# Performance work log

Hardware: AMD Instinct MI355X
Metric: run time of the kernel (lower is better)

Reference implementation:

```python
import jax, jax.numpy as jnp
import numpy as np

B, N, E = 4, 50000, 800000
C_IN, C_OUT, OUT = 64, 64, 32


def _uniform(key, shape, fan_in):
    s = 1.0 / np.sqrt(fan_in)
    return jax.random.uniform(key, shape, jnp.float32, -s, s)


def setup_inputs() -> dict:
    key = jax.random.key(0)
    ks = jax.random.split(key, 16)
    x = jax.random.normal(ks[0], (B, N, C_IN), jnp.float32)
    edge_index = jax.random.randint(ks[1], (2, E), 0, N, jnp.int64)
    edge_weight = jax.random.uniform(ks[2], (E,), jnp.float32)
    # GCNConv weights (in->out) and biases for z, r, h gates
    Wz = _uniform(ks[3], (C_IN, C_OUT), C_IN); bz = jnp.zeros((C_OUT,), jnp.float32)
    Wr = _uniform(ks[4], (C_IN, C_OUT), C_IN); br = jnp.zeros((C_OUT,), jnp.float32)
    Wh = _uniform(ks[5], (C_IN, C_OUT), C_IN); bh = jnp.zeros((C_OUT,), jnp.float32)
    # gating Linears: (2*out -> out)
    Lz = _uniform(ks[6], (2 * C_OUT, C_OUT), 2 * C_OUT); Lzb = _uniform(ks[7], (C_OUT,), 2 * C_OUT)
    Lr = _uniform(ks[8], (2 * C_OUT, C_OUT), 2 * C_OUT); Lrb = _uniform(ks[9], (C_OUT,), 2 * C_OUT)
    Lh = _uniform(ks[10], (2 * C_OUT, C_OUT), 2 * C_OUT); Lhb = _uniform(ks[11], (C_OUT,), 2 * C_OUT)
    # output head Linear(out_channels -> out_size)
    Hw = _uniform(ks[12], (C_OUT, OUT), C_OUT); Hb = _uniform(ks[13], (OUT,), C_OUT)
    return dict(x=x, edge_index=edge_index, edge_weight=edge_weight,
                Wz=Wz, bz=bz, Wr=Wr, br=br, Wh=Wh, bh=bh,
                Lz=Lz, Lzb=Lzb, Lr=Lr, Lrb=Lrb, Lh=Lh, Lhb=Lhb,
                Hw=Hw, Hb=Hb)


def _gcn(x, W, b, src, tgt, norm):
    # x: (B, N, Cin) -> (B, N, Cout); sym-normalized aggregation over edges
    xw = jnp.einsum('bnf,fo->bno', x, W)
    msg = xw[:, src] * norm[None, :, None]          # (B, E+N, Cout)
    agg = jnp.zeros_like(xw).at[:, tgt].add(msg)    # scatter-add at targets
    return agg + b


def reference(x, edge_index, edge_weight, Wz, bz, Wr, br, Wh, bh,
              Lz, Lzb, Lr, Lrb, Lh, Lhb, Hw, Hb):
    src, tgt = edge_index[0], edge_index[1]
    loop = jnp.arange(N)
    src_f = jnp.concatenate([src, loop])
    tgt_f = jnp.concatenate([tgt, loop])
    w_f = jnp.concatenate([edge_weight, jnp.ones((N,), edge_weight.dtype)])
    deg = jnp.zeros((N,), w_f.dtype).at[tgt_f].add(w_f)  # self-loops => deg >= 1
    dinv = jax.lax.rsqrt(deg)
    norm = dinv[src_f] * w_f * dinv[tgt_f]
    H = jnp.zeros((x.shape[0], N, Wz.shape[1]), x.dtype)  # TGCN2 initial hidden state
    gz = _gcn(x, Wz, bz, src_f, tgt_f, norm)
    Z = jax.nn.sigmoid(jnp.concatenate([gz, H], -1) @ Lz + Lzb)
    gr = _gcn(x, Wr, br, src_f, tgt_f, norm)
    R = jax.nn.sigmoid(jnp.concatenate([gr, H], -1) @ Lr + Lrb)
    gh = _gcn(x, Wh, bh, src_f, tgt_f, norm)
    Ht = jnp.tanh(jnp.concatenate([gh, H * R], -1) @ Lh + Lhb)
    Hn = Z * H + (1.0 - Z) * Ht
    return jax.nn.relu(Hn) @ Hw + Hb
```

## Files before the change

### kernel.cpp

```cpp
#include <hip/hip_runtime.h>
#include <stdint.h>

#define N_NODES 50000
#define N_EDGES 800000
#define XSTRIDE 3200000
#define PS      3200000
#define PSU     1600000
#define EBLK    3125
#define XPBLK   12500
#define FUSE_T  15730
#define MAXDEG  64
#define CSH     24
#define WMASK   0xFFFFFFu

typedef __attribute__((ext_vector_type(8))) short short8;
typedef __attribute__((ext_vector_type(4))) float float4v;

static __device__ __forceinline__ unsigned f2bf(float f) {
  unsigned u = __float_as_uint(f);
  return (u + 0x7fffu + ((u >> 16) & 1u)) >> 16;
}
static __device__ __forceinline__ float bflo(unsigned u) { return __uint_as_float(u << 16); }
static __device__ __forceinline__ float bfhi(unsigned u) { return __uint_as_float(u & 0xffff0000u); }
static __device__ __forceinline__ float dinv_of(unsigned pk) {
  return rsqrtf(1.0f + (float)(pk & WMASK) * 0x1p-18f);
}

__global__ __launch_bounds__(256) void kfused(
    const float* __restrict__ x, uint2* __restrict__ xp,
    const int* __restrict__ tgt, const int* __restrict__ src,
    const float* __restrict__ ew,
    unsigned* __restrict__ packed32, int2* __restrict__ colw,
    const float* __restrict__ Wz, const float* __restrict__ bz,
    const float* __restrict__ Wh, const float* __restrict__ bh,
    const float* __restrict__ Lz, const float* __restrict__ Lzb,
    const float* __restrict__ Lh, const float* __restrict__ Lhb,
    const float* __restrict__ Hw,
    ushort* __restrict__ BG, ushort* __restrict__ BH, float* __restrict__ czh) {
  int blk = blockIdx.x;
  if (blk % 5 == 0) {
    int eb = blk / 5;
    if (eb >= EBLK) return;
    int e = eb * 256 + threadIdx.x;
    int t = tgt[e], s = src[e];
    t = t < 0 ? 0 : (t >= N_NODES ? N_NODES - 1 : t);
    s = s < 0 ? 0 : (s >= N_NODES ? N_NODES - 1 : s);
    float wv = ew[e];
    wv = wv < 0.f ? 0.f : wv;
    unsigned fix = (unsigned)(wv * 262144.0f);
    fix = fix > 262143u ? 262143u : fix;
    unsigned old = atomicAdd(&packed32[t], (1u << CSH) | fix);
    unsigned rank = old >> CSH;
    if (rank < MAXDEG)
      colw[t * MAXDEG + (int)rank] = make_int2(s, __float_as_int(wv));
    return;
  }
  int j = blk - blk / 5 - 1;
  if (j < XPBLK) {
    int i = j * 256 + threadIdx.x;
    float v0 = x[i];
    float v1 = x[i + XSTRIDE];
    float v2 = x[i + 2 * XSTRIDE];
    float v3 = x[i + 3 * XSTRIDE];
    uint2 u;
    u.x = (f2bf(v1) << 16) | f2bf(v0);
    u.y = (f2bf(v3) << 16) | f2bf(v2);
    xp[i] = u;
    return;
  }
  int idx = (j - XPBLK) * 256 + threadIdx.x;
  if (idx < 16384) {
    int i = idx & 7, lane = (idx >> 3) & 63, kk = (idx >> 9) & 1;
    int jt = (idx >> 10) & 7, hilo = idx >> 13;
    int c = kk * 32 + ((lane >> 4) << 3) + i;
    int jj0 = jt * 16 + (lane & 15);
    const float* W = (jj0 < 64) ? Wz : Wh;
    const float* L = (jj0 < 64) ? Lz : Lh;
    int jj = jj0 & 63;
    float v = 0.f;
    #pragma unroll 8
    for (int k = 0; k < 64; ++k) v += W[c * 64 + k] * L[k * 64 + jj];
    unsigned hi = f2bf(v);
    BG[idx] = hilo ? (ushort)f2bf(v - bflo(hi)) : (ushort)hi;
  } else if (idx < 20480) {
    int t = idx - 16384;
    int i = t & 7, lane = (t >> 3) & 63, kk = (t >> 9) & 1;
    int ot = (t >> 10) & 1, hilo = (t >> 11) & 1;
    int c = kk * 32 + ((lane >> 4) << 3) + i;
    int o = ot * 16 + (lane & 15);
    float v = Hw[c * 32 + o];
    unsigned hi = f2bf(v);
    BH[t] = hilo ? (ushort)f2bf(v - bflo(hi)) : (ushort)hi;
  } else if (idx < 20608) {
    int jj0 = idx - 20480;
    int jj = jj0 & 63;
    const float* L  = (jj0 < 64) ? Lz  : Lh;
    const float* bb = (jj0 < 64) ? bz  : bh;
    const float* Lb = (jj0 < 64) ? Lzb : Lhb;
    float v = Lb[jj];
    #pragma unroll 8
    for (int k = 0; k < 64; ++k) v += bb[k] * L[k * 64 + jj];
    czh[jj0] = v;
  }
}

__global__ __launch_bounds__(256) void kagg(
    const uint4* __restrict__ xp4, const unsigned* __restrict__ packed32,
    const int4* __restrict__ colw4, unsigned* __restrict__ aggp32) {
  int lane = threadIdx.x & 63;
  int w = threadIdx.x >> 6;
  int n = blockIdx.x * 4 + w;
  int c2 = lane & 31;
  int eh = lane >> 5;
  unsigned pk = packed32[n];
  int cnt = (int)(pk >> CSH);
  cnt = cnt > MAXDEG ? MAXDEG : cnt;
  float dinv_n = dinv_of(pk);
  float a0, a1, a2, a3, b0, b1, b2, b3;
  {
    float g = eh ? 0.0f : dinv_n;
    uint4 q = xp4[(size_t)n * 32 + c2];
    a0 = g * bflo(q.x); a1 = g * bfhi(q.x);
    a2 = g * bflo(q.y); a3 = g * bfhi(q.y);
    b0 = g * bflo(q.z); b1 = g * bfhi(q.z);
    b2 = g * bflo(q.w); b3 = g * bfhi(q.w);
  }
  const int4* row = colw4 + (size_t)n * (MAXDEG / 2);
  const int2* row2 = (const int2*)row;
  int p = 0;
  for (; p + 8 <= cnt; p += 8) {
    int4 m0 = row[(p >> 1) + 2 * eh];
    int4 m1 = row[(p >> 1) + 2 * eh + 1];
    float w0 = __int_as_float(m0.y) * dinv_of(packed32[m0.x]);
    float w1 = __int_as_float(m0.w) * dinv_of(packed32[m0.z]);
    float w2 = __int_as_float(m1.y) * dinv_of(packed32[m1.x]);
    float w3 = __int_as_float(m1.w) * dinv_of(packed32[m1.z]);
    uint4 q0 = xp4[(size_t)m0.x * 32 + c2];
    uint4 q1 = xp4[(size_t)m0.z * 32 + c2];
    uint4 q2 = xp4[(size_t)m1.x * 32 + c2];
    uint4 q3 = xp4[(size_t)m1.z * 32 + c2];
    a0 += w0*bflo(q0.x) + w1*bflo(q1.x) + w2*bflo(q2.x) + w3*bflo(q3.x);
    a1 += w0*bfhi(q0.x) + w1*bfhi(q1.x) + w2*bfhi(q2.x) + w3*bfhi(q3.x);
    a2 += w0*bflo(q0.y) + w1*bflo(q1.y) + w2*bflo(q2.y) + w3*bflo(q3.y);
    a3 += w0*bfhi(q0.y) + w1*bfhi(q1.y) + w2*bfhi(q2.y) + w3*bfhi(q3.y);
    b0 += w0*bflo(q0.z) + w1*bflo(q1.z) + w2*bflo(q2.z) + w3*bflo(q3.z);
    b1 += w0*bfhi(q0.z) + w1*bfhi(q1.z) + w2*bfhi(q2.z) + w3*bfhi(q3.z);
    b2 += w0*bflo(q0.w) + w1*bflo(q1.w) + w2*bflo(q2.w) + w3*bflo(q3.w);
    b3 += w0*bfhi(q0.w) + w1*bfhi(q1.w) + w2*bfhi(q2.w) + w3*bfhi(q3.w);
  }
  for (; p + 2 <= cnt; p += 2) {
    int2 m = row2[p + eh];
    float wv = __int_as_float(m.y) * dinv_of(packed32[m.x]);
    uint4 q = xp4[(size_t)m.x * 32 + c2];
    a0 += wv * bflo(q.x); a1 += wv * bfhi(q.x);
    a2 += wv * bflo(q.y); a3 += wv * bfhi(q.y);
    b0 += wv * bflo(q.z); b1 += wv * bfhi(q.z);
    b2 += wv * bflo(q.w); b3 += wv * bfhi(q.w);
  }
  if (p < cnt) {
    int2 m = row2[p];
    float wv = eh ? 0.0f : __int_as_float(m.y) * dinv_of(packed32[m.x]);
    uint4 q = xp4[(size_t)m.x * 32 + c2];
    a0 += wv * bflo(q.x); a1 += wv * bfhi(q.x);
    a2 += wv * bflo(q.y); a3 += wv * bfhi(q.y);
    b0 += wv * bflo(q.z); b1 += wv * bfhi(q.z);
    b2 += wv * bflo(q.w); b3 += wv * bfhi(q.w);
  }
  a0 += __shfl_xor(a0, 32, 64); a1 += __shfl_xor(a1, 32, 64);
  a2 += __shfl_xor(a2, 32, 64); a3 += __shfl_xor(a3, 32, 64);
  b0 += __shfl_xor(b0, 32, 64); b1 += __shfl_xor(b1, 32, 64);
  b2 += __shfl_xor(b2, 32, 64); b3 += __shfl_xor(b3, 32, 64);
  float pa = dinv_n * (eh ? a2 : a0), pb = dinv_n * (eh ? b2 : b0);
  float qa = dinv_n * (eh ? a3 : a1), qb = dinv_n * (eh ? b3 : b1);
  unsigned vlo = f2bf(pa) | (f2bf(pb) << 16);
  unsigned vhi = f2bf(qa) | (f2bf(qb) << 16);
  size_t base = (size_t)(eh * 2) * PSU + (size_t)n * 32 + c2;
  aggp32[base]       = vlo;
  aggp32[base + PSU] = vhi;
}

__global__ __launch_bounds__(256) void kdense(
    const ushort* __restrict__ aggp,
    const ushort* __restrict__ BG, const ushort* __restrict__ BH,
    const float* __restrict__ czh, const float* __restrict__ Hb,
    float* __restrict__ out) {
  __shared__ uint4 sBGv[2048];
  __shared__ uint4 sBHv[512];
  __shared__ float sCzh[128];
  __shared__ float sHb[32];
  __shared__ uint4 sRv[4][128];

  int tid = threadIdx.x;
  {
    const uint4* g = (const uint4*)BG;
    for (int i = tid; i < 2048; i += 256) sBGv[i] = g[i];
    const uint4* g2 = (const uint4*)BH;
    for (int i = tid; i < 512; i += 256) sBHv[i] = g2[i];
    if (tid < 128) sCzh[tid] = czh[tid];
    if (tid < 32) sHb[tid] = Hb[tid];
  }
  __syncthreads();

  int lane = tid & 63;
  int w = tid >> 6;
  const short8* bgf = (const short8*)sBGv;
  const short8* bhf = (const short8*)sBHv;
  char* rbase = (char*)(&sRv[w][0]);
  int rowg = (lane >> 4) * 4;
  int colb = lane & 15;

  #pragma unroll 1
  for (int it = 0; it < 5; ++it) {
    int tile = (it * 625 + blockIdx.x) * 4 + w;
    int b = tile / 3125;
    int n0 = (tile - b * 3125) * 16;

    const ushort* ap = aggp + (size_t)b * PS + (size_t)(n0 + (lane & 15)) * 64
                       + ((lane >> 4) << 3);
    short8 a0 = *(const short8*)(ap);
    short8 a1 = *(const short8*)(ap + 32);

    float4v acc[8];
    #pragma unroll
    for (int jt = 0; jt < 8; ++jt) {
      float bias = sCzh[jt * 16 + (lane & 15)];
      acc[jt] = (float4v){bias, bias, bias, bias};
    }
    #pragma unroll
    for (int hilo = 0; hilo < 2; ++hilo) {
      #pragma unroll
      for (int jt = 0; jt < 8; ++jt) {
        short8 b0 = bgf[((hilo * 8 + jt) * 2 + 0) * 64 + lane];
        short8 b1 = bgf[((hilo * 8 + jt) * 2 + 1) * 64 + lane];
        acc[jt] = __builtin_amdgcn_mfma_f32_16x16x32_bf16(a0, b0, acc[jt], 0, 0, 0);
        acc[jt] = __builtin_amdgcn_mfma_f32_16x16x32_bf16(a1, b1, acc[jt], 0, 0, 0);
      }
    }

    #pragma unroll
    for (int jt = 0; jt < 4; ++jt) {
      #pragma unroll
      for (int r = 0; r < 4; ++r) {
        float z = acc[jt][r], h = acc[jt + 4][r];
        float s = 1.f / (1.f + __expf(-z));
        float e = __expf(2.f * h);
        float t = (e - 1.f) / (e + 1.f);
        float rr = (1.f - s) * t;
        rr = rr > 0.f ? rr : 0.f;
        int row = rowg + r;
        int colx = jt * 16 + colb;
        int byte = (row * 128 + colx * 2) ^ ((row & 7) << 4);
        *(ushort*)(rbase + byte) = (ushort)f2bf(rr);
      }
    }
    __syncthreads();

    short8 ra0, ra1;
    {
      int row = lane & 15;
      int g = (lane >> 4) << 4;
      int swz = (row & 7) << 4;
      ra0 = *(const short8*)(rbase + row * 128 + ((g) ^ swz));
      ra1 = *(const short8*)(rbase + row * 128 + ((64 + g) ^ swz));
    }
    float4v hacc[2];
    #pragma unroll
    for (int ot = 0; ot < 2; ++ot) {
      float hb = sHb[ot * 16 + (lane & 15)];
      hacc[ot] = (float4v){hb, hb, hb, hb};
    }
    #pragma unroll
    for (int hilo = 0; hilo < 2; ++hilo) {
      #pragma unroll
      for (int ot = 0; ot < 2; ++ot) {
        short8 b0 = bhf[((hilo * 2 + ot) * 2 + 0) * 64 + lane];
        short8 b1 = bhf[((hilo * 2 + ot) * 2 + 1) * 64 + lane];
        hacc[ot] = __builtin_amdgcn_mfma_f32_16x16x32_bf16(ra0, b0, hacc[ot], 0, 0, 0);
        hacc[ot] = __builtin_amdgcn_mfma_f32_16x16x32_bf16(ra1, b1, hacc[ot], 0, 0, 0);
      }
    }
    float* ob = out + ((size_t)b * N_NODES + n0) * 32;
    #pragma unroll
    for (int ot = 0; ot < 2; ++ot) {
      #pragma unroll
      for (int r = 0; r < 4; ++r) {
        int row = rowg + r;
        int o = ot * 16 + (lane & 15);
        ob[row * 32 + o] = hacc[ot][r];
      }
    }
    __syncthreads();
  }
}

extern "C" void kernel_launch(void* const* d_in, const int* in_sizes, int n_in,
                              void* d_out, int out_size, void* d_ws, size_t ws_size,
                              hipStream_t stream) {
  const float* x   = (const float*)d_in[0];
  const int*   ei  = (const int*)d_in[1];
  const float* ew  = (const float*)d_in[2];
  const float* Wz  = (const float*)d_in[3];
  const float* bz  = (const float*)d_in[4];
  const float* Wh  = (const float*)d_in[7];
  const float* bh  = (const float*)d_in[8];
  const float* Lz  = (const float*)d_in[9];
  const float* Lzb = (const float*)d_in[10];
  const float* Lh  = (const float*)d_in[13];
  const float* Lhb = (const float*)d_in[14];
  const float* Hw  = (const float*)d_in[15];
  const float* Hb  = (const float*)d_in[16];
  float* out = (float*)d_out;

  const int* src = ei;
  const int* tgt = ei + N_EDGES;

  char* ws = (char*)d_ws;
  ws = (char*)(((uintptr_t)ws + 255) & ~(uintptr_t)255);
  unsigned* packed32 = (unsigned*)ws; ws += (size_t)N_NODES * 4;
  ws = (char*)(((uintptr_t)ws + 255) & ~(uintptr_t)255);
  int2* colw = (int2*)ws;      ws += (size_t)N_NODES * MAXDEG * 8;
  ushort* BG    = (ushort*)ws; ws += 16384 * 2;
  ushort* BH    = (ushort*)ws; ws += 4096 * 2;
  float* czh    = (float*)ws;  ws += 128 * 4;
  ws = (char*)(((uintptr_t)ws + 255) & ~(uintptr_t)255);
  uint2* xp     = (uint2*)ws;  ws += (size_t)N_NODES * 64 * 8;
  unsigned* aggp32 = (unsigned*)ws; ws += (size_t)4 * PSU * 4;

  hipMemsetAsync(packed32, 0, (size_t)N_NODES * 4, stream);
  kfused<<<FUSE_T, 256, 0, stream>>>(
      x, xp, tgt, src, ew, packed32, colw,
      Wz, bz, Wh, bh, Lz, Lzb, Lh, Lhb, Hw, BG, BH, czh);
  kagg<<<N_NODES / 4, 256, 0, stream>>>((const uint4*)xp, packed32,
                                        (const int4*)colw, aggp32);
  kdense<<<625, 256, 0, stream>>>((const ushort*)aggp32, BG, BH, czh, Hb, out);
}
```

Measured before the change: 144.5 us.

## Slice node features into channel planes and gather 16 edges per wave

The packed bf16 features are rewritten into 8 channel-slice planes, so each aggregation block touches only one slice, a smaller gather footprint. The neighbour list is compressed to 4 bytes per edge: a 16-bit source index plus an fp16 weight. The aggregation kernel becomes a grid-stride loop in which each wave processes 16 edges at a time with 4 lanes per edge, reduced by xor shuffles. The aim is better cache locality and fewer index bytes, at the cost of more loop iterations and shuffles per node and reduced precision for edge weights.

```diff
diff --git a/kernel.cpp b/kernel.cpp
--- a/kernel.cpp
+++ b/kernel.cpp
@@ -1,4 +1,5 @@
 #include <hip/hip_runtime.h>
+#include <hip/hip_fp16.h>
 #include <stdint.h>
 
 #define N_NODES 50000
@@ -12,6 +13,10 @@
 #define MAXDEG  64
 #define CSH     24
 #define WMASK   0xFFFFFFu
+#define PLANE2  400000
+#define PLANE4  200000
+#define KAGG_B  12496
+#define WPS     6248
 
 typedef __attribute__((ext_vector_type(8))) short short8;
 typedef __attribute__((ext_vector_type(4))) float float4v;
@@ -27,10 +32,10 @@
 }
 
 __global__ __launch_bounds__(256) void kfused(
-    const float* __restrict__ x, uint2* __restrict__ xp,
+    const float* __restrict__ x, uint2* __restrict__ xps2,
     const int* __restrict__ tgt, const int* __restrict__ src,
     const float* __restrict__ ew,
-    unsigned* __restrict__ packed32, int2* __restrict__ colw,
+    unsigned* __restrict__ packed32, unsigned* __restrict__ colw,
     const float* __restrict__ Wz, const float* __restrict__ bz,
     const float* __restrict__ Wh, const float* __restrict__ bh,
     const float* __restrict__ Lz, const float* __restrict__ Lzb,
@@ -51,13 +56,16 @@
     fix = fix > 262143u ? 262143u : fix;
     unsigned old = atomicAdd(&packed32[t], (1u << CSH) | fix);
     unsigned rank = old >> CSH;
-    if (rank < MAXDEG)
-      colw[t * MAXDEG + (int)rank] = make_int2(s, __float_as_int(wv));
+    if (rank < MAXDEG) {
+      unsigned hb = (unsigned)__half_as_ushort(__float2half(wv));
+      colw[t * MAXDEG + (int)rank] = (hb << 16) | (unsigned)s;
+    }
     return;
   }
   int j = blk - blk / 5 - 1;
   if (j < XPBLK) {
     int i = j * 256 + threadIdx.x;
+    int n = i >> 6, ch = i & 63;
     float v0 = x[i];
     float v1 = x[i + XSTRIDE];
     float v2 = x[i + 2 * XSTRIDE];
@@ -65,7 +73,7 @@
     uint2 u;
     u.x = (f2bf(v1) << 16) | f2bf(v0);
     u.y = (f2bf(v3) << 16) | f2bf(v2);
-    xp[i] = u;
+    xps2[(ch >> 3) * PLANE2 + n * 8 + (ch & 7)] = u;
     return;
   }
   int idx = (j - XPBLK) * 256 + threadIdx.x;
@@ -105,78 +113,64 @@
 }
 
 __global__ __launch_bounds__(256) void kagg(
-    const uint4* __restrict__ xp4, const unsigned* __restrict__ packed32,
-    const int4* __restrict__ colw4, unsigned* __restrict__ aggp32) {
+    const uint4* __restrict__ xps4, const unsigned* __restrict__ packed32,
+    const unsigned* __restrict__ colw, unsigned* __restrict__ aggp32) {
   int lane = threadIdx.x & 63;
-  int w = threadIdx.x >> 6;
-  int n = blockIdx.x * 4 + w;
-  int c2 = lane & 31;
-  int eh = lane >> 5;
-  unsigned pk = packed32[n];
-  int cnt = (int)(pk >> CSH);
-  cnt = cnt > MAXDEG ? MAXDEG : cnt;
-  float dinv_n = dinv_of(pk);
-  float a0, a1, a2, a3, b0, b1, b2, b3;
-  {
-    float g = eh ? 0.0f : dinv_n;
-    uint4 q = xp4[(size_t)n * 32 + c2];
-    a0 = g * bflo(q.x); a1 = g * bfhi(q.x);
-    a2 = g * bflo(q.y); a3 = g * bfhi(q.y);
-    b0 = g * bflo(q.z); b1 = g * bfhi(q.z);
-    b2 = g * bflo(q.w); b3 = g * bfhi(q.w);
-  }
-  const int4* row = colw4 + (size_t)n * (MAXDEG / 2);
-  const int2* row2 = (const int2*)row;
-  int p = 0;
-  for (; p + 8 <= cnt; p += 8) {
-    int4 m0 = row[(p >> 1) + 2 * eh];
-    int4 m1 = row[(p >> 1) + 2 * eh + 1];
-    float w0 = __int_as_float(m0.y) * dinv_of(packed32[m0.x]);
-    float w1 = __int_as_float(m0.w) * dinv_of(packed32[m0.z]);
-    float w2 = __int_as_float(m1.y) * dinv_of(packed32[m1.x]);
-    float w3 = __int_as_float(m1.w) * dinv_of(packed32[m1.z]);
-    uint4 q0 = xp4[(size_t)m0.x * 32 + c2];
-    uint4 q1 = xp4[(size_t)m0.z * 32 + c2];
-    uint4 q2 = xp4[(size_t)m1.x * 32 + c2];
-    uint4 q3 = xp4[(size_t)m1.z * 32 + c2];
-    a0 += w0*bflo(q0.x) + w1*bflo(q1.x) + w2*bflo(q2.x) + w3*bflo(q3.x);
-    a1 += w0*bfhi(q0.x) + w1*bfhi(q1.x) + w2*bfhi(q2.x) + w3*bfhi(q3.x);
-    a2 += w0*bflo(q0.y) + w1*bflo(q1.y) + w2*bflo(q2.y) + w3*bflo(q3.y);
-    a3 += w0*bfhi(q0.y) + w1*bfhi(q1.y) + w2*bfhi(q2.y) + w3*bfhi(q3.y);
-    b0 += w0*bflo(q0.z) + w1*bflo(q1.z) + w2*bflo(q2.z) + w3*bflo(q3.z);
-    b1 += w0*bfhi(q0.z) + w1*bfhi(q1.z) + w2*bfhi(q2.z) + w3*bfhi(q3.z);
-    b2 += w0*bflo(q0.w) + w1*bflo(q1.w) + w2*bflo(q2.w) + w3*bflo(q3.w);
-    b3 += w0*bfhi(q0.w) + w1*bfhi(q1.w) + w2*bfhi(q2.w) + w3*bfhi(q3.w);
-  }
-  for (; p + 2 <= cnt; p += 2) {
-    int2 m = row2[p + eh];
-    float wv = __int_as_float(m.y) * dinv_of(packed32[m.x]);
-    uint4 q = xp4[(size_t)m.x * 32 + c2];
-    a0 += wv * bflo(q.x); a1 += wv * bfhi(q.x);
-    a2 += wv * bflo(q.y); a3 += wv * bfhi(q.y);
-    b0 += wv * bflo(q.z); b1 += wv * bfhi(q.z);
-    b2 += wv * bflo(q.w); b3 += wv * bfhi(q.w);
-  }
-  if (p < cnt) {
-    int2 m = row2[p];
-    float wv = eh ? 0.0f : __int_as_float(m.y) * dinv_of(packed32[m.x]);
-    uint4 q = xp4[(size_t)m.x * 32 + c2];
-    a0 += wv * bflo(q.x); a1 += wv * bfhi(q.x);
-    a2 += wv * bflo(q.y); a3 += wv * bfhi(q.y);
-    b0 += wv * bflo(q.z); b1 += wv * bfhi(q.z);
-    b2 += wv * bflo(q.w); b3 += wv * bfhi(q.w);
-  }
-  a0 += __shfl_xor(a0, 32, 64); a1 += __shfl_xor(a1, 32, 64);
-  a2 += __shfl_xor(a2, 32, 64); a3 += __shfl_xor(a3, 32, 64);
-  b0 += __shfl_xor(b0, 32, 64); b1 += __shfl_xor(b1, 32, 64);
-  b2 += __shfl_xor(b2, 32, 64); b3 += __shfl_xor(b3, 32, 64);
-  float pa = dinv_n * (eh ? a2 : a0), pb = dinv_n * (eh ? b2 : b0);
-  float qa = dinv_n * (eh ? a3 : a1), qb = dinv_n * (eh ? b3 : b1);
-  unsigned vlo = f2bf(pa) | (f2bf(pb) << 16);
-  unsigned vhi = f2bf(qa) | (f2bf(qb) << 16);
-  size_t base = (size_t)(eh * 2) * PSU + (size_t)n * 32 + c2;
-  aggp32[base]       = vlo;
-  aggp32[base + PSU] = vhi;
+  int wid = threadIdx.x >> 6;
+  int slice = blockIdx.x & 7;
+  int wave = (blockIdx.x >> 3) * 4 + wid;
+  int g = lane >> 2, q = lane & 3;
+  const uint4* plane = xps4 + (size_t)slice * PLANE4;
+
+  for (int n = wave; n < N_NODES; n += WPS) {
+    unsigned pk = packed32[n];
+    int cnt = (int)(pk >> CSH);
+    cnt = cnt > MAXDEG ? MAXDEG : cnt;
+    float dinv_n = dinv_of(pk);
+    float a0, a1, a2, a3, b0, b1, b2, b3;
+    {
+      float g0 = (g == 0) ? dinv_n : 0.0f;
+      uint4 qv = plane[n * 4 + q];
+      a0 = g0 * bflo(qv.x); a1 = g0 * bfhi(qv.x);
+      a2 = g0 * bflo(qv.y); a3 = g0 * bfhi(qv.y);
+      b0 = g0 * bflo(qv.z); b1 = g0 * bfhi(qv.z);
+      b2 = g0 * bflo(qv.w); b3 = g0 * bfhi(qv.w);
+    }
+    for (int c0 = 0; c0 < cnt; c0 += 16) {
+      int e = c0 + g;
+      bool valid = e < cnt;
+      unsigned m = valid ? __builtin_nontemporal_load(&colw[n * MAXDEG + e]) : 0u;
+      int s = (int)(m & 0xFFFFu);
+      float wv = 0.0f;
+      if (valid) {
+        wv = __half2float(__ushort_as_half((unsigned short)(m >> 16)))
+             * dinv_of(packed32[s]);
+      }
+      uint4 qv = plane[(size_t)s * 4 + q];
+      a0 += wv * bflo(qv.x); a1 += wv * bfhi(qv.x);
+      a2 += wv * bflo(qv.y); a3 += wv * bfhi(qv.y);
+      b0 += wv * bflo(qv.z); b1 += wv * bfhi(qv.z);
+      b2 += wv * bflo(qv.w); b3 += wv * bfhi(qv.w);
+    }
+    #pragma unroll
+    for (int mask = 4; mask <= 32; mask <<= 1) {
+      a0 += __shfl_xor(a0, mask, 64); a1 += __shfl_xor(a1, mask, 64);
+      a2 += __shfl_xor(a2, mask, 64); a3 += __shfl_xor(a3, mask, 64);
+      b0 += __shfl_xor(b0, mask, 64); b1 += __shfl_xor(b1, mask, 64);
+      b2 += __shfl_xor(b2, mask, 64); b3 += __shfl_xor(b3, mask, 64);
+    }
+    if (lane < 16) {
+      int p = lane >> 2;
+      float ea, eb;
+      if      (p == 0) { ea = a0; eb = b0; }
+      else if (p == 1) { ea = a1; eb = b1; }
+      else if (p == 2) { ea = a2; eb = b2; }
+      else             { ea = a3; eb = b3; }
+      ea *= dinv_n; eb *= dinv_n;
+      aggp32[(size_t)p * PSU + n * 32 + slice * 4 + q] =
+          f2bf(ea) | (f2bf(eb) << 16);
+    }
+  }
 }
 
 __global__ __launch_bounds__(256) void kdense(
@@ -318,19 +312,18 @@
   ws = (char*)(((uintptr_t)ws + 255) & ~(uintptr_t)255);
   unsigned* packed32 = (unsigned*)ws; ws += (size_t)N_NODES * 4;
   ws = (char*)(((uintptr_t)ws + 255) & ~(uintptr_t)255);
-  int2* colw = (int2*)ws;      ws += (size_t)N_NODES * MAXDEG * 8;
+  unsigned* colw = (unsigned*)ws; ws += (size_t)N_NODES * MAXDEG * 4;
   ushort* BG    = (ushort*)ws; ws += 16384 * 2;
   ushort* BH    = (ushort*)ws; ws += 4096 * 2;
   float* czh    = (float*)ws;  ws += 128 * 4;
   ws = (char*)(((uintptr_t)ws + 255) & ~(uintptr_t)255);
-  uint2* xp     = (uint2*)ws;  ws += (size_t)N_NODES * 64 * 8;
+  uint2* xps    = (uint2*)ws;  ws += (size_t)N_NODES * 64 * 8;
   unsigned* aggp32 = (unsigned*)ws; ws += (size_t)4 * PSU * 4;
 
   hipMemsetAsync(packed32, 0, (size_t)N_NODES * 4, stream);
   kfused<<<FUSE_T, 256, 0, stream>>>(
-      x, xp, tgt, src, ew, packed32, colw,
+      x, xps, tgt, src, ew, packed32, colw,
       Wz, bz, Wh, bh, Lz, Lzb, Lh, Lhb, Hw, BG, BH, czh);
-  kagg<<<N_NODES / 4, 256, 0, stream>>>((const uint4*)xp, packed32,
-                                        (const int4*)colw, aggp32);
+  kagg<<<KAGG_B, 256, 0, stream>>>((const uint4*)xps, packed32, colw, aggp32);
   kdense<<<625, 256, 0, stream>>>((const ushort*)aggp32, BG, BH, czh, Hb, out);
 }
```

After: 276.3 us. 1.91x slower.
